# Performance work log

Measured on AMD Instinct MI355X. Metric: run time of the kernel, lower is better.

Reference implementation:

```python
import math
import jax, jax.numpy as jnp
import numpy as np

DIM, NHEAD, TOPK = 512, 8, 64
DK = DIM // NHEAD
B, T = 4, 2048


def setup_inputs() -> dict:
    key = jax.random.key(0)
    k1, k2, k3 = jax.random.split(key, 3)
    x = jax.random.normal(k1, (B, T, DIM), jnp.float32)
    # qkv Linear (bias=False): represent as [dim, 3*dim] so y = x @ Wqkv
    Wqkv = jax.random.normal(k2, (DIM, 3 * DIM), jnp.float32) * (DIM ** -0.5)
    Wout = jax.random.normal(k3, (DIM, DIM), jnp.float32) * (DIM ** -0.5)
    alpha = jnp.zeros((NHEAD,), jnp.float32)  # nn.Parameter(torch.zeros(nhead))
    return {"x": x, "Wqkv": Wqkv, "Wout": Wout, "alpha": alpha}


def reference(x, Wqkv, Wout, alpha):
    Bx, Tx, C = x.shape
    H, dk, k = NHEAD, DK, TOPK

    qkv = x @ Wqkv  # [B,T,3C]
    q, kk, v = jnp.split(qkv, 3, axis=-1)
    to_heads = lambda t: t.reshape(Bx, Tx, H, dk).transpose(0, 2, 1, 3)  # [B,H,T,dk]
    q, kk, v = to_heads(q), to_heads(kk), to_heads(v)

    attn = jnp.einsum('bhtd,bhsd->bhts', q, kk) / math.sqrt(dk)  # [B,H,T,T]
    dense = jnp.einsum('bhts,bhsd->bhtd', jax.nn.softmax(attn, axis=-1), v)

    # top-k mask along last axis (topk < T in this config)
    idx = jax.lax.top_k(attn, k)[1]                       # [B,H,T,k]
    a2 = attn.reshape(-1, Tx)
    i2 = idx.reshape(-1, k)
    row = jnp.arange(a2.shape[0])[:, None]
    keep = jnp.zeros(a2.shape, jnp.bool_).at[row, i2].set(True).reshape(attn.shape)
    masked = jnp.where(keep, attn, jnp.float32(-1e9))     # masked_fill(mask, -1e9)
    sparse = jnp.einsum('bhts,bhsd->bhtd', jax.nn.softmax(masked, axis=-1), v)

    gate = jax.nn.sigmoid(alpha).reshape(1, H, 1, 1)
    out = (gate * dense + (1.0 - gate) * sparse).transpose(0, 2, 1, 3).reshape(Bx, Tx, C)
    return out @ Wout
```

## Files before the change

### kernel.cpp

```cpp
#include <hip/hip_runtime.h>
#include <hip/hip_bf16.h>
#include <cstdint>
#include <cstddef>


#define TSEQ 2048

typedef __attribute__((ext_vector_type(8))) short bf8;
typedef __attribute__((ext_vector_type(4))) float f32x4;

#define MFMA16(A, B, C) \
  C = __builtin_amdgcn_mfma_f32_16x16x32_bf16(A, B, C, 0, 0, 0)

static __device__ __forceinline__ short f2bf(float f) {
  unsigned u = __float_as_uint(f);
  u += 0x7FFFu + ((u >> 16) & 1u);
  return (short)(u >> 16);
}
static __device__ __forceinline__ float bf2f(short s) {
  return __uint_as_float(((unsigned)(unsigned short)s) << 16);
}
static __device__ __forceinline__ unsigned pack_bf16x2(float a, float b) {
  float2 f2; f2.x = a; f2.y = b;
  __hip_bfloat162 h = __float22bfloat162_rn(f2);
  unsigned r;
  __builtin_memcpy(&r, &h, 4);
  return r;
}

__global__ __launch_bounds__(256) void transpose_split(
    const float* __restrict__ W, short* __restrict__ out, int K, int N) {
  __shared__ float tile[32][129];
  const int t = threadIdx.x;
  const int nb = blockIdx.x * 128, kb = blockIdx.y * 32;
#pragma unroll
  for (int c = 0; c < 4; ++c) {
    const int flat = c * 256 + t;
    const int r = flat >> 5, nq = (flat & 31) * 4;
    const float4 g = *reinterpret_cast<const float4*>(&W[(size_t)(kb + r) * N + nb + nq]);
    tile[r][nq] = g.x; tile[r][nq + 1] = g.y;
    tile[r][nq + 2] = g.z; tile[r][nq + 3] = g.w;
  }
  __syncthreads();
  const int n = t >> 1, kh = (t & 1) * 16;
  bf8 a0, a1, b0, b1;
#pragma unroll
  for (int e = 0; e < 16; ++e) {
    const float f = tile[kh + e][n];
    const short s1 = f2bf(f);
    const short s2 = f2bf(f - bf2f(s1));
    if (e < 8) { a0[e] = s1; b0[e] = s2; }
    else       { a1[e - 8] = s1; b1[e - 8] = s2; }
  }
  const size_t o = (size_t)(nb + n) * K + kb + kh;
  const size_t ls = (size_t)N * K;
  *reinterpret_cast<bf8*>(out + o) = a0;
  *reinterpret_cast<bf8*>(out + o + 8) = a1;
  *reinterpret_cast<bf8*>(out + o + ls) = b0;
  *reinterpret_cast<bf8*>(out + o + ls + 8) = b1;
}

__global__ __launch_bounds__(256) void transpose_split3(
    const float* __restrict__ W, short* __restrict__ out, int K, int N) {
  __shared__ float tile[32][129];
  const int t = threadIdx.x;
  const int nb = blockIdx.x * 128, kb = blockIdx.y * 32;
#pragma unroll
  for (int c = 0; c < 4; ++c) {
    const int flat = c * 256 + t;
    const int r = flat >> 5, nq = (flat & 31) * 4;
    const float4 g = *reinterpret_cast<const float4*>(&W[(size_t)(kb + r) * N + nb + nq]);
    tile[r][nq] = g.x; tile[r][nq + 1] = g.y;
    tile[r][nq + 2] = g.z; tile[r][nq + 3] = g.w;
  }
  __syncthreads();
  const int n = t >> 1, kh = (t & 1) * 16;
  bf8 a0, a1, b0, b1, c0, c1;
#pragma unroll
  for (int e = 0; e < 16; ++e) {
    const float f = tile[kh + e][n];
    const short s1 = f2bf(f);  const float r1 = f - bf2f(s1);
    const short s2 = f2bf(r1);
    const short s3 = f2bf(r1 - bf2f(s2));
    if (e < 8) { a0[e] = s1; b0[e] = s2; c0[e] = s3; }
    else       { a1[e - 8] = s1; b1[e - 8] = s2; c1[e - 8] = s3; }
  }
  const size_t o = (size_t)(nb + n) * K + kb + kh;
  const size_t ls = (size_t)N * K;
  *reinterpret_cast<bf8*>(out + o) = a0;
  *reinterpret_cast<bf8*>(out + o + 8) = a1;
  *reinterpret_cast<bf8*>(out + o + ls) = b0;
  *reinterpret_cast<bf8*>(out + o + ls + 8) = b1;
  *reinterpret_cast<bf8*>(out + o + 2 * ls) = c0;
  *reinterpret_cast<bf8*>(out + o + 2 * ls + 8) = c1;
}

__global__ __launch_bounds__(256) void xsplit3(
    const float* __restrict__ X, short* __restrict__ XS) {
  const int i = (blockIdx.x * 256 + threadIdx.x) * 8;
  const float4 g0 = *reinterpret_cast<const float4*>(X + i);
  const float4 g1 = *reinterpret_cast<const float4*>(X + i + 4);
  const float v[8] = {g0.x, g0.y, g0.z, g0.w, g1.x, g1.y, g1.z, g1.w};
  bf8 s1v, s2v, s3v;
#pragma unroll
  for (int e = 0; e < 8; ++e) {
    const short s1 = f2bf(v[e]);  const float r1 = v[e] - bf2f(s1);
    const short s2 = f2bf(r1);
    const short s3 = f2bf(r1 - bf2f(s2));
    s1v[e] = s1; s2v[e] = s2; s3v[e] = s3;
  }
  *reinterpret_cast<bf8*>(XS + i)           = s1v;
  *reinterpret_cast<bf8*>(XS + i + 4194304) = s2v;
  *reinterpret_cast<bf8*>(XS + i + 8388608) = s3v;
}

__global__ __launch_bounds__(256) void qkv_gemm(
    const float* __restrict__ X, const float* __restrict__ W,
    float* __restrict__ Qf32, short* __restrict__ KF, short* __restrict__ VF) {
  __shared__ float As[16][132];
  __shared__ float Bs[16][132];
  const int t = threadIdx.x;
  const int n0 = blockIdx.x * 128;
  const int m0 = blockIdx.y * 128;
  const int ti = t >> 4, tj = t & 15;
  float acc[8][8] = {};
  for (int kt = 0; kt < 512; kt += 16) {
#pragma unroll
    for (int e = 0; e < 2; ++e) {
      int idx = e * 256 + t;
      int m = idx >> 2, kq = (idx & 3) << 2;
      const float4 g = *reinterpret_cast<const float4*>(
          &X[(size_t)(m0 + m) * 512 + kt + kq]);
      As[kq + 0][m] = g.x; As[kq + 1][m] = g.y;
      As[kq + 2][m] = g.z; As[kq + 3][m] = g.w;
    }
#pragma unroll
    for (int e = 0; e < 2; ++e) {
      int idx = e * 256 + t;
      int kk = idx >> 5, n4 = (idx & 31) << 2;
      *reinterpret_cast<float4*>(&Bs[kk][n4]) =
          *reinterpret_cast<const float4*>(&W[(size_t)(kt + kk) * 1536 + n0 + n4]);
    }
    __syncthreads();
#pragma unroll
    for (int kk = 0; kk < 16; ++kk) {
      const float4 A0 = *reinterpret_cast<const float4*>(&As[kk][ti * 8]);
      const float4 A1 = *reinterpret_cast<const float4*>(&As[kk][ti * 8 + 4]);
      const float4 B0 = *reinterpret_cast<const float4*>(&Bs[kk][tj * 8]);
      const float4 B1 = *reinterpret_cast<const float4*>(&Bs[kk][tj * 8 + 4]);
      const float a[8] = {A0.x, A0.y, A0.z, A0.w, A1.x, A1.y, A1.z, A1.w};
      const float b[8] = {B0.x, B0.y, B0.z, B0.w, B1.x, B1.y, B1.z, B1.w};
#pragma unroll
      for (int ii = 0; ii < 8; ++ii)
#pragma unroll
        for (int jj = 0; jj < 8; ++jj)
          acc[ii][jj] = fmaf(a[ii], b[jj], acc[ii][jj]);
    }
    __syncthreads();
  }
  const int part = n0 >> 9;
  if (part == 0) {
#pragma unroll
    for (int ii = 0; ii < 8; ++ii) {
      const int r = m0 + ti * 8 + ii;
      const int bb = r >> 11, tt = r & 2047;
#pragma unroll
      for (int jj = 0; jj < 8; ++jj) {
        const int c = (n0 & 511) + tj * 8 + jj;
        const int h = c >> 6, d = c & 63;
        Qf32[(size_t)(bb * 8 + h) * 131072 + (size_t)tt * 64 + d] =
            acc[ii][jj] * 0.125f;
      }
    }
  } else if (part == 1) {
    const int cc0 = (n0 & 511) + tj * 8;
    const int h = cc0 >> 6, d0 = cc0 & 63;
    const int kk = d0 >> 5, lg = (d0 & 31) >> 3;
#pragma unroll
    for (int ii = 0; ii < 8; ++ii) {
      const int r = m0 + ti * 8 + ii;
      const int bb = r >> 11, tt = r & 2047;
      const size_t base = (size_t)(bb * 8 + h) * 393216 +
                          (size_t)(tt >> 4) * 3072 + kk * 512 +
                          ((tt & 15) + 16 * lg) * 8;
      bf8 v1, v2, v3;
#pragma unroll
      for (int jj = 0; jj < 8; ++jj) {
        const float f = acc[ii][jj];
        const short s1 = f2bf(f);  const float r1 = f - bf2f(s1);
        const short s2 = f2bf(r1);
        const short s3 = f2bf(r1 - bf2f(s2));
        v1[jj] = s1; v2[jj] = s2; v3[jj] = s3;
      }
      *reinterpret_cast<bf8*>(KF + base)        = v1;
      *reinterpret_cast<bf8*>(KF + base + 1024) = v2;
      *reinterpret_cast<bf8*>(KF + base + 2048) = v3;
    }
  } else {
    const int t0r = m0 + ti * 8;
    const int bb = t0r >> 11, tt0 = t0r & 2047;
    const int cc = tt0 >> 5, lgs = (tt0 & 31) >> 3;
#pragma unroll
    for (int jj = 0; jj < 8; ++jj) {
      const int c = (n0 & 511) + tj * 8 + jj;
      const int h = c >> 6, dd = c & 63;
      bf8 pv;
#pragma unroll
      for (int ii = 0; ii < 8; ++ii) pv[ii] = f2bf(acc[ii][jj]);
      *reinterpret_cast<bf8*>(VF + (size_t)(bb * 8 + h) * 131072 +
                              cc * 2048 + (dd >> 4) * 512 +
                              ((dd & 15) + 16 * lgs) * 8) = pv;
    }
  }
}

__global__ __launch_bounds__(256) void qkv_mfma(
    const short* __restrict__ XS, const short* __restrict__ WqS,
    float* __restrict__ Qf32, short* __restrict__ KF, short* __restrict__ VF) {
  extern __shared__ char sm_[];
  short* As = (short*)sm_;
  short* Bs = (short*)(sm_ + 30720);
  float* SC = (float*)sm_;
  const int t = threadIdx.x;
  const int w = t >> 6, lane = t & 63;
  const int lq = lane & 15, lg = lane >> 4;
  const int wr = w >> 1, wc = w & 1;
  const int n0 = blockIdx.x * 128, m0 = blockIdx.y * 128;
  const int part = n0 >> 9;
  f32x4 acc[4][4];
#pragma unroll
  for (int i = 0; i < 4; ++i)
#pragma unroll
    for (int j2 = 0; j2 < 4; ++j2) acc[i][j2] = (f32x4){0.f, 0.f, 0.f, 0.f};
  const int sr = t >> 1, sh = (t & 1) * 16;
  for (int k0 = 0; k0 < 512; k0 += 32) {
#pragma unroll
    for (int lev = 0; lev < 3; ++lev) {
      const size_t xa = (size_t)lev * 4194304 + (size_t)(m0 + sr) * 512 + k0 + sh;
      *reinterpret_cast<bf8*>(&As[(lev * 128 + sr) * 40 + sh])     =
          *reinterpret_cast<const bf8*>(XS + xa);
      *reinterpret_cast<bf8*>(&As[(lev * 128 + sr) * 40 + sh + 8]) =
          *reinterpret_cast<const bf8*>(XS + xa + 8);
      const size_t wa = (size_t)lev * 786432 + (size_t)(n0 + sr) * 512 + k0 + sh;
      *reinterpret_cast<bf8*>(&Bs[(lev * 128 + sr) * 40 + sh])     =
          *reinterpret_cast<const bf8*>(WqS + wa);
      *reinterpret_cast<bf8*>(&Bs[(lev * 128 + sr) * 40 + sh + 8]) =
          *reinterpret_cast<const bf8*>(WqS + wa + 8);
    }
    __syncthreads();
    bf8 bfr[4][3];
#pragma unroll
    for (int i = 0; i < 4; ++i)
#pragma unroll
      for (int lev = 0; lev < 3; ++lev)
        bfr[i][lev] = *reinterpret_cast<const bf8*>(
            &Bs[(lev * 128 + wc * 64 + i * 16 + lq) * 40 + lg * 8]);
#pragma unroll
    for (int mi = 0; mi < 4; ++mi) {
      bf8 af0 = *reinterpret_cast<const bf8*>(
          &As[(0 * 128 + wr * 64 + mi * 16 + lq) * 40 + lg * 8]);
      bf8 af1 = *reinterpret_cast<const bf8*>(
          &As[(1 * 128 + wr * 64 + mi * 16 + lq) * 40 + lg * 8]);
      bf8 af2 = *reinterpret_cast<const bf8*>(
          &As[(2 * 128 + wr * 64 + mi * 16 + lq) * 40 + lg * 8]);
#pragma unroll
      for (int ni = 0; ni < 4; ++ni) {
        MFMA16(af0, bfr[ni][0], acc[mi][ni]);
        MFMA16(af0, bfr[ni][1], acc[mi][ni]);
        MFMA16(af1, bfr[ni][0], acc[mi][ni]);
        MFMA16(af1, bfr[ni][1], acc[mi][ni]);
        MFMA16(af0, bfr[ni][2], acc[mi][ni]);
        MFMA16(af2, bfr[ni][0], acc[mi][ni]);
      }
    }
    __syncthreads();
  }
#pragma unroll
  for (int mi = 0; mi < 4; ++mi)
#pragma unroll
    for (int ni = 0; ni < 4; ++ni)
#pragma unroll
      for (int r = 0; r < 4; ++r)
        SC[(wr * 64 + mi * 16 + lg * 4 + r) * 132 + wc * 64 + ni * 16 + lq] =
            acc[mi][ni][r];
  __syncthreads();
  const int ti = t >> 4, tj = t & 15;
  float accL[8][8];
#pragma unroll
  for (int ii = 0; ii < 8; ++ii) {
    const float4 c0 = *reinterpret_cast<const float4*>(&SC[(ti * 8 + ii) * 132 + tj * 8]);
    const float4 c1 = *reinterpret_cast<const float4*>(&SC[(ti * 8 + ii) * 132 + tj * 8 + 4]);
    accL[ii][0] = c0.x; accL[ii][1] = c0.y; accL[ii][2] = c0.z; accL[ii][3] = c0.w;
    accL[ii][4] = c1.x; accL[ii][5] = c1.y; accL[ii][6] = c1.z; accL[ii][7] = c1.w;
  }
  if (part == 0) {
#pragma unroll
    for (int ii = 0; ii < 8; ++ii) {
      const int r = m0 + ti * 8 + ii;
      const int bb = r >> 11, tt = r & 2047;
#pragma unroll
      for (int jj = 0; jj < 8; ++jj) {
        const int c = (n0 & 511) + tj * 8 + jj;
        const int h = c >> 6, d = c & 63;
        Qf32[(size_t)(bb * 8 + h) * 131072 + (size_t)tt * 64 + d] =
            accL[ii][jj] * 0.125f;
      }
    }
  } else if (part == 1) {
    const int cc0 = (n0 & 511) + tj * 8;
    const int h = cc0 >> 6, d0 = cc0 & 63;
    const int kk = d0 >> 5, lg2 = (d0 & 31) >> 3;
#pragma unroll
    for (int ii = 0; ii < 8; ++ii) {
      const int r = m0 + ti * 8 + ii;
      const int bb = r >> 11, tt = r & 2047;
      const size_t base = (size_t)(bb * 8 + h) * 393216 +
                          (size_t)(tt >> 4) * 3072 + kk * 512 +
                          ((tt & 15) + 16 * lg2) * 8;
      bf8 v1, v2, v3;
#pragma unroll
      for (int jj = 0; jj < 8; ++jj) {
        const float f = accL[ii][jj];
        const short s1 = f2bf(f);  const float r1 = f - bf2f(s1);
        const short s2 = f2bf(r1);
        const short s3 = f2bf(r1 - bf2f(s2));
        v1[jj] = s1; v2[jj] = s2; v3[jj] = s3;
      }
      *reinterpret_cast<bf8*>(KF + base)        = v1;
      *reinterpret_cast<bf8*>(KF + base + 1024) = v2;
      *reinterpret_cast<bf8*>(KF + base + 2048) = v3;
    }
  } else {
    const int t0r = m0 + ti * 8;
    const int bb = t0r >> 11, tt0 = t0r & 2047;
    const int cc = tt0 >> 5, lgs = (tt0 & 31) >> 3;
#pragma unroll
    for (int jj = 0; jj < 8; ++jj) {
      const int c = (n0 & 511) + tj * 8 + jj;
      const int h = c >> 6, dd = c & 63;
      bf8 pv;
#pragma unroll
      for (int ii = 0; ii < 8; ++ii) pv[ii] = f2bf(accL[ii][jj]);
      *reinterpret_cast<bf8*>(VF + (size_t)(bb * 8 + h) * 131072 +
                              cc * 2048 + (dd >> 4) * 512 +
                              ((dd & 15) + 16 * lgs) * 8) = pv;
    }
  }
}

__global__ __launch_bounds__(256) void out_mfma(
    const short* __restrict__ HOS, const short* __restrict__ WoS,
    float* __restrict__ OUT) {
  __shared__ short As[2][128][40];
  __shared__ short Bs[2][128][40];
  const int t = threadIdx.x;
  const int w = t >> 6, lane = t & 63;
  const int lq = lane & 15, lg = lane >> 4;
  const int wr = w >> 1, wc = w & 1;
  const int n0 = blockIdx.x * 128, m0 = blockIdx.y * 128;
  f32x4 acc[4][4];
#pragma unroll
  for (int i = 0; i < 4; ++i)
#pragma unroll
    for (int j2 = 0; j2 < 4; ++j2) acc[i][j2] = (f32x4){0.f, 0.f, 0.f, 0.f};
  const int sm = t >> 1, sh = (t & 1) * 16;
  for (int k0 = 0; k0 < 512; k0 += 32) {
#pragma unroll
    for (int lev = 0; lev < 2; ++lev) {
      const size_t xa = (size_t)lev * 4194304 + (size_t)(m0 + sm) * 512 + k0 + sh;
      *reinterpret_cast<bf8*>(&As[lev][sm][sh])     = *reinterpret_cast<const bf8*>(HOS + xa);
      *reinterpret_cast<bf8*>(&As[lev][sm][sh + 8]) = *reinterpret_cast<const bf8*>(HOS + xa + 8);
      const size_t wa = (size_t)lev * 262144 + (size_t)(n0 + sm) * 512 + k0 + sh;
      *reinterpret_cast<bf8*>(&Bs[lev][sm][sh])     = *reinterpret_cast<const bf8*>(WoS + wa);
      *reinterpret_cast<bf8*>(&Bs[lev][sm][sh + 8]) = *reinterpret_cast<const bf8*>(WoS + wa + 8);
    }
    __syncthreads();
    bf8 af[4][2], bfr[4][2];
#pragma unroll
    for (int i = 0; i < 4; ++i)
#pragma unroll
      for (int lev = 0; lev < 2; ++lev) {
        af[i][lev]  = *reinterpret_cast<const bf8*>(&As[lev][wr * 64 + i * 16 + lq][lg * 8]);
        bfr[i][lev] = *reinterpret_cast<const bf8*>(&Bs[lev][wc * 64 + i * 16 + lq][lg * 8]);
      }
#pragma unroll
    for (int mi = 0; mi < 4; ++mi)
#pragma unroll
      for (int ni = 0; ni < 4; ++ni) {
        MFMA16(af[mi][0], bfr[ni][0], acc[mi][ni]);
        MFMA16(af[mi][0], bfr[ni][1], acc[mi][ni]);
        MFMA16(af[mi][1], bfr[ni][0], acc[mi][ni]);
      }
    __syncthreads();
  }
#pragma unroll
  for (int mi = 0; mi < 4; ++mi)
#pragma unroll
    for (int r = 0; r < 4; ++r) {
      const int m = m0 + wr * 64 + mi * 16 + lg * 4 + r;
#pragma unroll
      for (int ni = 0; ni < 4; ++ni)
        OUT[(size_t)m * 512 + n0 + wc * 64 + ni * 16 + lq] = acc[mi][ni][r];
    }
}

__global__ __launch_bounds__(512, 4) void attn_mfma(
    const float* __restrict__ Qf32, const short* __restrict__ KF,
    const short* __restrict__ VF, const float* __restrict__ alpha,
    short* __restrict__ HOS) {
  extern __shared__ char lds[];
  const int tid = threadIdx.x;
  const int w = tid >> 6, lane = tid & 63;
  const int lq = lane & 15, lg = lane >> 4;
  const int row = lq;

  const int flat = blockIdx.x + (int)gridDim.x * blockIdx.y;
  const int xcd = flat & 7, idx = flat >> 3;
  const int bh = xcd * 4 + (idx >> 7);
  const int qb = idx & 127;
  const int b = bh >> 3, h = bh & 7;
  const int q0 = qb * 16;

  const float gate = 1.0f / (1.0f + __expf(-alpha[h]));
  const int key = row & 7;

  bf8 qf[3][2];
  {
    const float* qp = Qf32 + (size_t)bh * 131072 + (size_t)(q0 + row) * 64 + lg * 8;
#pragma unroll
    for (int kk = 0; kk < 2; ++kk) {
      const float4 g0 = *reinterpret_cast<const float4*>(qp + kk * 32);
      const float4 g1 = *reinterpret_cast<const float4*>(qp + kk * 32 + 4);
      const float v[8] = {g0.x, g0.y, g0.z, g0.w, g1.x, g1.y, g1.z, g1.w};
#pragma unroll
      for (int e = 0; e < 8; ++e) {
        const short s1 = f2bf(v[e]);  const float r1 = v[e] - bf2f(s1);
        const short s2 = f2bf(r1);
        const short s3 = f2bf(r1 - bf2f(s2));
        qf[0][kk][e] = s1; qf[1][kk][e] = s2; qf[2][kk][e] = s3;
      }
    }
  }

  auto ldk = [&](int t, bf8 (&dst)[3][2]) {
    const short* p = KF + (size_t)(bh * 128 + t) * 3072 + lane * 8;
    dst[0][0] = *reinterpret_cast<const bf8*>(p);
    dst[0][1] = *reinterpret_cast<const bf8*>(p + 512);
    dst[1][0] = *reinterpret_cast<const bf8*>(p + 1024);
    dst[1][1] = *reinterpret_cast<const bf8*>(p + 1536);
    dst[2][0] = *reinterpret_cast<const bf8*>(p + 2048);
    dst[2][1] = *reinterpret_cast<const bf8*>(p + 2560);
  };
  auto qk = [&](bf8 (&kf)[3][2], int t) {
    f32x4 c0 = {0.f,0.f,0.f,0.f}, c1 = {0.f,0.f,0.f,0.f}, c2 = {0.f,0.f,0.f,0.f};
#pragma unroll
    for (int kk = 0; kk < 2; ++kk) {
      MFMA16(kf[0][kk], qf[0][kk], c0);
      MFMA16(kf[0][kk], qf[1][kk], c1);
      MFMA16(kf[1][kk], qf[0][kk], c1);
      MFMA16(kf[1][kk], qf[1][kk], c2);
      MFMA16(kf[0][kk], qf[2][kk], c2);
      MFMA16(kf[2][kk], qf[0][kk], c2);
    }
    const f32x4 c = (c0 + c1) + c2;
    *reinterpret_cast<f32x4*>(
        lds + row * 4096 + ((((((t & 63) << 2)) + lg) ^ key) << 4)) = c;
  };

  float av[2][32];
  float lm[2] = {-3.402823466e+38f, -3.402823466e+38f};

  bf8 ka[3][2], kb[3][2];
  ldk(w, ka);
#pragma unroll
  for (int j = 0; j < 8; j += 2) {
    const int t0 = w + 8 * j;
    ldk(t0 + 8, kb);
    qk(ka, t0);
    if (j + 2 < 8) ldk(t0 + 16, ka);
    qk(kb, t0 + 8);
  }
  ldk(w + 64, ka);
  __syncthreads();

#pragma unroll
  for (int rr = 0; rr < 2; ++rr) {
    const char* rowb = lds + (w + 8 * rr) * 4096;
#pragma unroll
    for (int jj = 0; jj < 4; ++jj) {
      const f32x4 v = *reinterpret_cast<const f32x4*>(rowb + ((lane + 64 * jj) << 4));
#pragma unroll
      for (int e = 0; e < 4; ++e) {
        av[rr][jj * 4 + e] = v[e];
        lm[rr] = fmaxf(lm[rr], v[e]);
      }
    }
  }
  __syncthreads();

#pragma unroll
  for (int j = 0; j < 8; j += 2) {
    const int t0 = 64 + w + 8 * j;
    ldk(t0 + 8, kb);
    qk(ka, t0);
    if (j + 2 < 8) ldk(t0 + 16, ka);
    qk(kb, t0 + 8);
  }
  __syncthreads();

  const int dt3 = w & 3, cg = w >> 2;
  bf8 va1, vb1;
  auto ldv1 = [&](int cc, bf8& dst) {
    dst = *reinterpret_cast<const bf8*>(
        VF + (size_t)(bh * 64 + cc) * 2048 + dt3 * 512 + lane * 8);
  };
  {
#pragma unroll
    for (int rr = 0; rr < 2; ++rr) {
      const char* rowb = lds + (w + 8 * rr) * 4096;
#pragma unroll
      for (int jj = 4; jj < 8; ++jj) {
        const f32x4 v = *reinterpret_cast<const f32x4*>(
            rowb + ((lane + 64 * (jj - 4)) << 4));
#pragma unroll
        for (int e = 0; e < 4; ++e) {
          av[rr][jj * 4 + e] = v[e];
          lm[rr] = fmaxf(lm[rr], v[e]);
        }
      }
    }
    ldv1(cg * 32, va1);
#pragma unroll
    for (int rr = 0; rr < 2; ++rr) {
      const int q = w + 8 * rr;
      const int rkey = q & 7;
      float m = lm[rr], g0 = lm[rr];
#pragma unroll
      for (int off = 32; off; off >>= 1) {
        m = fmaxf(m, __shfl_xor(m, off));
        g0 = fminf(g0, __shfl_xor(g0, off));
      }
      float lo = g0, hi = m;
      for (int it = 0; it < 64; ++it) {
        const float mid = 0.5f * (lo + hi);
        if (!(mid > lo && mid < hi)) break;
        int cnt = 0;
#pragma unroll
        for (int j = 0; j < 32; ++j)
          cnt += (int)__popcll(__ballot(av[rr][j] >= mid));
        if (cnt >= 64) {
          lo = mid;
          if (cnt == 64) break;
        } else {
          hi = mid;
        }
      }
      const float thr = lo;
      float dsum = 0.f, ssum = 0.f;
#pragma unroll
      for (int j = 0; j < 32; ++j) {
        const float e = __expf(av[rr][j] - m);
        dsum += e;
        ssum += (av[rr][j] >= thr) ? e : 0.f;
      }
#pragma unroll
      for (int off = 32; off; off >>= 1) {
        dsum += __shfl_xor(dsum, off);
        ssum += __shfl_xor(ssum, off);
      }
      const float dinv = gate / dsum;
      const float sinv = (1.0f - gate) / ssum;
#pragma unroll
      for (int jj = 0; jj < 8; ++jj) {
        const int p = lane + 64 * jj;
        const int f = p ^ rkey;
        float wv[4];
#pragma unroll
        for (int e2 = 0; e2 < 4; ++e2) {
          const float a = av[rr][jj * 4 + e2];
          wv[e2] = __expf(a - m) * (dinv + ((a >= thr) ? sinv : 0.f));
        }
        uint2 pk;
        pk.x = pack_bf16x2(wv[0], wv[1]);
        pk.y = pack_bf16x2(wv[2], wv[3]);
        *reinterpret_cast<uint2*>(
            lds + q * 4096 + ((((f >> 1) ^ rkey) << 4) + ((f & 1) << 3))) = pk;
      }
    }
  }
  __syncthreads();

  f32x4 o = {0.f, 0.f, 0.f, 0.f};
  {
    auto pv1 = [&](bf8 vv, int cc) {
      const bf8 pa = *reinterpret_cast<const bf8*>(
          lds + row * 4096 + ((((cc << 2) + lg) ^ key) << 4));
      MFMA16(pa, vv, o);
    };
#pragma unroll
    for (int j = 0; j < 32; j += 2) {
      const int cc = cg * 32 + j;
      ldv1(cc + 1, vb1);
      pv1(va1, cc);
      if (j + 2 < 32) ldv1(cc + 2, va1);
      pv1(vb1, cc + 1);
    }
  }
  {
    char* pb = lds + 65536 + (w << 10);
#pragma unroll
    for (int r = 0; r < 4; ++r)
      *reinterpret_cast<float*>(pb + (((lg * 4 + r) * 16 + lq) << 2)) = o[r];
  }
  __syncthreads();
  {
#pragma unroll
    for (int p = 0; p < 2; ++p) {
      const int q = (tid >> 6) + 8 * p, d = tid & 63;
      const int dt2 = d >> 4;
      const float s =
          *reinterpret_cast<const float*>(
              lds + 65536 + (dt2 << 10) + ((q * 16 + (d & 15)) << 2)) +
          *reinterpret_cast<const float*>(
              lds + 65536 + ((4 + dt2) << 10) + ((q * 16 + (d & 15)) << 2));
      const size_t o2 = (size_t)(b * TSEQ + q0 + q) * 512 + h * 64 + d;
      const short s1 = f2bf(s);
      HOS[o2] = s1;
      HOS[o2 + 4194304] = f2bf(s - bf2f(s1));
    }
  }
}

extern "C" void kernel_launch(void* const* d_in, const int* in_sizes, int n_in,
                              void* d_out, int out_size, void* d_ws, size_t ws_size,
                              hipStream_t stream) {
  const float* x     = (const float*)d_in[0];
  const float* Wqkv  = (const float*)d_in[1];
  const float* Wout  = (const float*)d_in[2];
  const float* alpha = (const float*)d_in[3];
  float* out = (float*)d_out;

  float* Qf32 = (float*)d_ws;
  short* S16  = (short*)d_ws;
  short* KF   = S16 + 8388608;
  short* VF   = S16 + 20971520;
  short* HOS  = S16 + 25165824;
  short* WoS  = S16 + 33554432;
  short* WqS  = S16 + 34078720;
  short* XSp  = S16 + 36438016;

  const int attn_lds = 73728;
  (void)hipFuncSetAttribute((const void*)attn_mfma,
                            hipFuncAttributeMaxDynamicSharedMemorySize, attn_lds);

  transpose_split<<<dim3(4, 16), 256, 0, stream>>>(Wout, WoS, 512, 512);

  const bool big = ws_size >= (size_t)98041856;
  if (big) {
    transpose_split3<<<dim3(12, 16), 256, 0, stream>>>(Wqkv, WqS, 512, 1536);
    xsplit3<<<2048, 256, 0, stream>>>(x, XSp);
    const int qkv_lds = 67584;
    (void)hipFuncSetAttribute((const void*)qkv_mfma,
                              hipFuncAttributeMaxDynamicSharedMemorySize, qkv_lds);
    qkv_mfma<<<dim3(12, 64), 256, qkv_lds, stream>>>(XSp, WqS, Qf32, KF, VF);
  } else {
    qkv_gemm<<<dim3(12, 64), 256, 0, stream>>>(x, Wqkv, Qf32, KF, VF);
  }
  attn_mfma<<<dim3(128, 32), 512, attn_lds, stream>>>(Qf32, KF, VF, alpha, HOS);
  out_mfma<<<dim3(4, 64), 256, 0, stream>>>(HOS, WoS, out);
}
```

Measured before the change: 373.3 us.

## Use fewer split-bf16 levels for V projection and deepen V prefetch in attention

Splits the QKV projection into two launches. Q and K columns keep the three-level split-bf16 emulation of fp32, while V columns use only two levels (three MFMAs instead of six), which roughly halves the matrix work for that third. The attention kernel now prefetches V four chunks ahead through a rotating register ring instead of double buffering, and swaps launch_bounds min-blocks for an explicit waves_per_eu attribute. The lower V precision risks accuracy drift, and the extra launch adds overhead.

```diff
diff --git a/kernel.cpp b/kernel.cpp
--- a/kernel.cpp
+++ b/kernel.cpp
@@ -214,9 +214,11 @@
   }
 }
 
-__global__ __launch_bounds__(256) void qkv_mfma(
+template <int LV>
+__global__ __launch_bounds__(256) void qkv_mfma_t(
     const short* __restrict__ XS, const short* __restrict__ WqS,
-    float* __restrict__ Qf32, short* __restrict__ KF, short* __restrict__ VF) {
+    float* __restrict__ Qf32, short* __restrict__ KF, short* __restrict__ VF,
+    int nbase) {
   extern __shared__ char sm_[];
   short* As = (short*)sm_;
   short* Bs = (short*)(sm_ + 30720);
@@ -225,7 +227,7 @@
   const int w = t >> 6, lane = t & 63;
   const int lq = lane & 15, lg = lane >> 4;
   const int wr = w >> 1, wc = w & 1;
-  const int n0 = blockIdx.x * 128, m0 = blockIdx.y * 128;
+  const int n0 = nbase + blockIdx.x * 128, m0 = blockIdx.y * 128;
   const int part = n0 >> 9;
   f32x4 acc[4][4];
 #pragma unroll
@@ -235,7 +237,7 @@
   const int sr = t >> 1, sh = (t & 1) * 16;
   for (int k0 = 0; k0 < 512; k0 += 32) {
 #pragma unroll
-    for (int lev = 0; lev < 3; ++lev) {
+    for (int lev = 0; lev < LV; ++lev) {
       const size_t xa = (size_t)lev * 4194304 + (size_t)(m0 + sr) * 512 + k0 + sh;
       *reinterpret_cast<bf8*>(&As[(lev * 128 + sr) * 40 + sh])     =
           *reinterpret_cast<const bf8*>(XS + xa);
@@ -248,11 +250,11 @@
           *reinterpret_cast<const bf8*>(WqS + wa + 8);
     }
     __syncthreads();
-    bf8 bfr[4][3];
+    bf8 bfr[4][LV];
 #pragma unroll
     for (int i = 0; i < 4; ++i)
 #pragma unroll
-      for (int lev = 0; lev < 3; ++lev)
+      for (int lev = 0; lev < LV; ++lev)
         bfr[i][lev] = *reinterpret_cast<const bf8*>(
             &Bs[(lev * 128 + wc * 64 + i * 16 + lq) * 40 + lg * 8]);
 #pragma unroll
@@ -261,16 +263,20 @@
           &As[(0 * 128 + wr * 64 + mi * 16 + lq) * 40 + lg * 8]);
       bf8 af1 = *reinterpret_cast<const bf8*>(
           &As[(1 * 128 + wr * 64 + mi * 16 + lq) * 40 + lg * 8]);
-      bf8 af2 = *reinterpret_cast<const bf8*>(
-          &As[(2 * 128 + wr * 64 + mi * 16 + lq) * 40 + lg * 8]);
+      bf8 af2;
+      if constexpr (LV == 3)
+        af2 = *reinterpret_cast<const bf8*>(
+            &As[(2 * 128 + wr * 64 + mi * 16 + lq) * 40 + lg * 8]);
 #pragma unroll
       for (int ni = 0; ni < 4; ++ni) {
         MFMA16(af0, bfr[ni][0], acc[mi][ni]);
         MFMA16(af0, bfr[ni][1], acc[mi][ni]);
         MFMA16(af1, bfr[ni][0], acc[mi][ni]);
-        MFMA16(af1, bfr[ni][1], acc[mi][ni]);
-        MFMA16(af0, bfr[ni][2], acc[mi][ni]);
-        MFMA16(af2, bfr[ni][0], acc[mi][ni]);
+        if constexpr (LV == 3) {
+          MFMA16(af1, bfr[ni][1], acc[mi][ni]);
+          MFMA16(af0, bfr[ni][2], acc[mi][ni]);
+          MFMA16(af2, bfr[ni][0], acc[mi][ni]);
+        }
       }
     }
     __syncthreads();
@@ -404,7 +410,8 @@
     }
 }
 
-__global__ __launch_bounds__(512, 4) void attn_mfma(
+__global__ __launch_bounds__(512)
+__attribute__((amdgpu_waves_per_eu(4, 4))) void attn_mfma(
     const float* __restrict__ Qf32, const short* __restrict__ KF,
     const short* __restrict__ VF, const float* __restrict__ alpha,
     short* __restrict__ HOS) {
@@ -509,7 +516,7 @@
   __syncthreads();
 
   const int dt3 = w & 3, cg = w >> 2;
-  bf8 va1, vb1;
+  bf8 vv[4];
   auto ldv1 = [&](int cc, bf8& dst) {
     dst = *reinterpret_cast<const bf8*>(
         VF + (size_t)(bh * 64 + cc) * 2048 + dt3 * 512 + lane * 8);
@@ -529,7 +536,8 @@
         }
       }
     }
-    ldv1(cg * 32, va1);
+#pragma unroll
+    for (int k = 0; k < 4; ++k) ldv1(cg * 32 + k, vv[k]);
 #pragma unroll
     for (int rr = 0; rr < 2; ++rr) {
       const int q = w + 8 * rr;
@@ -592,18 +600,16 @@
 
   f32x4 o = {0.f, 0.f, 0.f, 0.f};
   {
-    auto pv1 = [&](bf8 vv, int cc) {
+    auto pv1 = [&](bf8 vvv, int cc) {
       const bf8 pa = *reinterpret_cast<const bf8*>(
           lds + row * 4096 + ((((cc << 2) + lg) ^ key) << 4));
-      MFMA16(pa, vv, o);
+      MFMA16(pa, vvv, o);
     };
 #pragma unroll
-    for (int j = 0; j < 32; j += 2) {
+    for (int j = 0; j < 32; ++j) {
       const int cc = cg * 32 + j;
-      ldv1(cc + 1, vb1);
-      pv1(va1, cc);
-      if (j + 2 < 32) ldv1(cc + 2, va1);
-      pv1(vb1, cc + 1);
+      pv1(vv[j & 3], cc);
+      if (j + 4 < 32) ldv1(cc + 4, vv[j & 3]);
     }
   }
   {
@@ -660,9 +666,12 @@
     transpose_split3<<<dim3(12, 16), 256, 0, stream>>>(Wqkv, WqS, 512, 1536);
     xsplit3<<<2048, 256, 0, stream>>>(x, XSp);
     const int qkv_lds = 67584;
-    (void)hipFuncSetAttribute((const void*)qkv_mfma,
+    (void)hipFuncSetAttribute((const void*)qkv_mfma_t<3>,
                               hipFuncAttributeMaxDynamicSharedMemorySize, qkv_lds);
-    qkv_mfma<<<dim3(12, 64), 256, qkv_lds, stream>>>(XSp, WqS, Qf32, KF, VF);
+    (void)hipFuncSetAttribute((const void*)qkv_mfma_t<2>,
+                              hipFuncAttributeMaxDynamicSharedMemorySize, qkv_lds);
+    qkv_mfma_t<3><<<dim3(8, 64), 256, qkv_lds, stream>>>(XSp, WqS, Qf32, KF, VF, 0);
+    qkv_mfma_t<2><<<dim3(4, 64), 256, qkv_lds, stream>>>(XSp, WqS, Qf32, KF, VF, 1024);
   } else {
     qkv_gemm<<<dim3(12, 64), 256, 0, stream>>>(x, Wqkv, Qf32, KF, VF);
   }
```

Measured after the change: 396.4 us. 6.2% more time.
